# Optimization experiments

Measured on AMD Instinct MI355X. Metric: run time of the kernel, lower is better.

The kernel has to match this reference:

```python
import jax, jax.numpy as jnp
import numpy as np

N_NODES = 50000
N_EDGES = 800000
IN_CH, HID_CH, OUT_CH = 128, 128, 64


def setup_inputs() -> dict:
    key = jax.random.key(0)
    k1, k2, k3, k4 = jax.random.split(key, 4)
    x = jax.random.normal(k1, (N_NODES, IN_CH), dtype=jnp.float32)
    edge_index = jax.random.randint(k2, (2, N_EDGES), 0, N_NODES, dtype=jnp.int64)
    W1 = jax.random.normal(k3, (IN_CH, HID_CH), dtype=jnp.float32) * (1.0 / np.sqrt(IN_CH))
    b1 = jnp.zeros((HID_CH,), dtype=jnp.float32)
    W2 = jax.random.normal(k4, (HID_CH, OUT_CH), dtype=jnp.float32) * (1.0 / np.sqrt(HID_CH))
    b2 = jnp.zeros((OUT_CH,), dtype=jnp.float32)
    return {"x": x, "edge_index": edge_index, "W1": W1, "b1": b1, "W2": W2, "b2": b2}


def _gcn_conv(x, src, dst, norm, W, b, n_nodes):
    # x' = D^-1/2 (A+I) D^-1/2 (x W) + b
    h = x @ W                                        # [N, C_out]
    msg = norm[:, None] * h[src]                     # gather + scale, [E', C_out]
    agg = jax.ops.segment_sum(msg, dst, num_segments=n_nodes)
    return agg + b


def reference(x, edge_index, W1, b1, W2, b2):
    n = x.shape[0]
    # add self loops
    loops = jnp.arange(n, dtype=edge_index.dtype)
    src = jnp.concatenate([edge_index[0], loops])
    dst = jnp.concatenate([edge_index[1], loops])
    # symmetric degree normalization computed on target index
    deg = jax.ops.segment_sum(jnp.ones_like(dst, dtype=x.dtype), dst, num_segments=n)
    dinv = jnp.where(deg > 0, jax.lax.rsqrt(deg), 0.0)
    norm = dinv[src] * dinv[dst]                     # [E']

    h = jax.nn.relu(_gcn_conv(x, src, dst, norm, W1, b1, n))
    logits = _gcn_conv(h, src, dst, norm, W2, b2, n)
    return jax.nn.softmax(logits, axis=1)
```

## Files before the change

### kernel.cpp

```cpp
#include <hip/hip_runtime.h>
#include <hip/hip_fp16.h>


#define SLOT 64
#define NB   49
#define CAP  18432
#define EPB  4096

typedef _Float16 h4 __attribute__((ext_vector_type(4)));
typedef _Float16 h8 __attribute__((ext_vector_type(8)));
typedef float f4 __attribute__((ext_vector_type(4)));

__global__ __launch_bounds__(256) void k_part(const int* __restrict__ ei,
                                              int* __restrict__ bcur,
                                              unsigned int* __restrict__ bkt,
                                              int e) {
    __shared__ int sSrc[EPB];
    __shared__ int sDst[EPB];
    __shared__ int sCnt[64];
    int b0 = blockIdx.x * EPB;
    int cnt = min(EPB, e - b0);
    for (int i = threadIdx.x; i < cnt; i += 256) {
        sSrc[i] = ei[b0 + i];
        sDst[i] = ei[e + b0 + i];
    }
    if (threadIdx.x < 64) sCnt[threadIdx.x] = 0;
    __syncthreads();
    for (int i = threadIdx.x; i < cnt; i += 256)
        atomicAdd(&sCnt[sDst[i] >> 10], 1);
    __syncthreads();
    if (threadIdx.x < 64) {
        int c = sCnt[threadIdx.x];
        int gbase = (c > 0 && threadIdx.x < NB) ? atomicAdd(&bcur[threadIdx.x], c) : 0;
        sCnt[threadIdx.x] = gbase;
    }
    __syncthreads();
    for (int i = threadIdx.x; i < cnt; i += 256) {
        int d = sDst[i];
        int b = d >> 10;
        int pos = atomicAdd(&sCnt[b], 1);
        if (pos < CAP)
            bkt[(size_t)b * CAP + pos] =
                ((unsigned int)(d & 1023) << 16) | (unsigned int)sSrc[i];
    }
}

__global__ __launch_bounds__(256) void k_build(const int* __restrict__ bcur,
                                               const unsigned int* __restrict__ bkt,
                                               unsigned short* __restrict__ csr,
                                               int* __restrict__ deg,
                                               float* __restrict__ dinv, int n) {
    __shared__ unsigned short rows[256 * SLOT];
    __shared__ int cur[256];
    int r = blockIdx.x;
    int b = r >> 2;
    int q = r & 3;
    cur[threadIdx.x] = 0;
    __syncthreads();
    int cnt = min(bcur[b], CAP);
    const unsigned int* bp = bkt + (size_t)b * CAP;
    for (int i = threadIdx.x; i < cnt; i += 256) {
        unsigned int p = bp[i];
        int dl = (int)(p >> 16);
        if ((dl >> 8) == q) {
            int node = dl & 255;
            int pos = atomicAdd(&cur[node], 1);
            if (pos < SLOT) rows[node * SLOT + pos] = (unsigned short)(p & 0xffff);
        }
    }
    __syncthreads();
    int base = r * 256;
    uint4* dst4 = (uint4*)(csr + (size_t)base * SLOT);
    const uint4* src4 = (const uint4*)rows;
    for (int i = threadIdx.x; i < 256 * SLOT / 8; i += 256) dst4[i] = src4[i];
    int node = base + threadIdx.x;
    if (node < n) {
        int c = cur[threadIdx.x];
        deg[node] = c;
        dinv[node] = rsqrtf((float)(c + 1));
    }
}

__global__ __launch_bounds__(256) void k_splitw(const float* __restrict__ W1,
                                                const float* __restrict__ W2,
                                                _Float16* __restrict__ W1p,
                                                _Float16* __restrict__ W2p) {
    int i = blockIdx.x * 256 + threadIdx.x;
    float w; int k, c; _Float16* dst;
    if (i < 16384)      { k = i >> 7, c = i & 127; w = W1[i]; dst = W1p; }
    else if (i < 24576) { int t = i - 16384; k = t >> 6; c = t & 63; w = W2[t]; dst = W2p; }
    else return;
    _Float16 hi = (_Float16)w;
    _Float16 lo = (_Float16)(w - (float)hi);
    int kc = k >> 4, kk = k & 15;
    int l = (kk >> 2) * 16 + (c & 15);
    int j = kk & 3;
    int ct = c >> 4;
    size_t base = ((size_t)(ct * 8 + kc) * 64 + l) * 8 + j;
    dst[base] = hi;
    dst[base + 4] = lo;
}

__global__ __launch_bounds__(256) void k_gemm1(
    const float* __restrict__ X, const _Float16* __restrict__ Wp,
    __half* __restrict__ H, int n)
{
    int w = threadIdx.x >> 6, lane = threadIdx.x & 63;
    int r0 = blockIdx.x * 64 + w * 16;
    int xr = r0 + (lane & 15);
    int xrc = min(xr, n - 1);
    const float* xp = X + (size_t)xrc * 128 + ((lane >> 4) * 4);

    f4 acc[8];
#pragma unroll
    for (int ct = 0; ct < 8; ++ct) acc[ct] = (f4){0.f, 0.f, 0.f, 0.f};

#pragma unroll
    for (int kc = 0; kc < 8; ++kc) {
        float4 xv = *(const float4*)(xp + kc * 16);
        h4 xh, xl;
        xh[0] = (_Float16)xv.x; xh[1] = (_Float16)xv.y;
        xh[2] = (_Float16)xv.z; xh[3] = (_Float16)xv.w;
        xl[0] = (_Float16)(xv.x - (float)xh[0]);
        xl[1] = (_Float16)(xv.y - (float)xh[1]);
        xl[2] = (_Float16)(xv.z - (float)xh[2]);
        xl[3] = (_Float16)(xv.w - (float)xh[3]);
#pragma unroll
        for (int ct = 0; ct < 8; ++ct) {
            h8 wb = ((const h8*)Wp)[(ct * 8 + kc) * 64 + lane];
            h4 wh = {wb[0], wb[1], wb[2], wb[3]};
            h4 wl = {wb[4], wb[5], wb[6], wb[7]};
            acc[ct] = __builtin_amdgcn_mfma_f32_16x16x16f16(wh, xh, acc[ct], 0, 0, 0);
            acc[ct] = __builtin_amdgcn_mfma_f32_16x16x16f16(wl, xh, acc[ct], 0, 0, 0);
            acc[ct] = __builtin_amdgcn_mfma_f32_16x16x16f16(wh, xl, acc[ct], 0, 0, 0);
        }
    }
    if (xr < n) {
        __half* hp = H + (size_t)xr * 128 + (lane >> 4) * 4;
#pragma unroll
        for (int ct = 0; ct < 8; ++ct) {
            h4 o = {(_Float16)acc[ct][0], (_Float16)acc[ct][1],
                    (_Float16)acc[ct][2], (_Float16)acc[ct][3]};
            *(h4*)(hp + ct * 16) = o;
        }
    }
}

__global__ __launch_bounds__(256) void k_agg1(
    const int* __restrict__ deg, const unsigned short* __restrict__ csr,
    const float* __restrict__ dinv, const __half* __restrict__ H,
    const float* __restrict__ b1, float* __restrict__ H1, int n)
{
    int node = blockIdx.x * 4 + (threadIdx.x >> 6);
    if (node >= n) return;
    int lane = threadIdx.x & 63;
    int g = lane >> 4, sub = lane & 15;
    float dd = dinv[node];

    float acc[8];
#pragma unroll
    for (int i = 0; i < 8; ++i) acc[i] = 0.f;

    int beg = node * SLOT;
    int cnt = min(deg[node], SLOT);
    {
        int m = cnt;
        int   s_l = (lane < m) ? (int)csr[beg + lane] : 0;
        float w_l = (lane < m) ? dinv[s_l] * dd : 0.f;
        int iters = (m + 3) >> 2;
#pragma unroll 4
        for (int t = 0; t < iters; ++t) {
            int j = 4 * t + g;
            int   s = __shfl(s_l, j);
            float w = __shfl(w_l, j);
            float4 raw = ((const float4*)(H + (size_t)s * 128))[sub];
            const __half2* h2 = (const __half2*)&raw;
#pragma unroll
            for (int q = 0; q < 4; ++q) {
                float2 v = __half22float2(h2[q]);
                acc[2 * q]     = fmaf(w, v.x, acc[2 * q]);
                acc[2 * q + 1] = fmaf(w, v.y, acc[2 * q + 1]);
            }
        }
    }
#pragma unroll
    for (int i = 0; i < 8; ++i) {
        acc[i] += __shfl_xor(acc[i], 16);
        acc[i] += __shfl_xor(acc[i], 32);
    }
    float4 sraw = ((const float4*)(H + (size_t)node * 128))[sub];
    const __half2* sh2 = (const __half2*)&sraw;
    float sl = dd * dd;
    float4 bb0 = ((const float4*)(b1 + sub * 8))[0];
    float4 bb1 = ((const float4*)(b1 + sub * 8))[1];
    float out[8];
#pragma unroll
    for (int q = 0; q < 4; ++q) {
        float2 v = __half22float2(sh2[q]);
        out[2 * q]     = fmaf(sl, v.x, acc[2 * q]);
        out[2 * q + 1] = fmaf(sl, v.y, acc[2 * q + 1]);
    }
    out[0] += bb0.x; out[1] += bb0.y; out[2] += bb0.z; out[3] += bb0.w;
    out[4] += bb1.x; out[5] += bb1.y; out[6] += bb1.z; out[7] += bb1.w;
#pragma unroll
    for (int i = 0; i < 8; ++i) out[i] = fmaxf(out[i], 0.f);
    float* op = H1 + (size_t)node * 128 + sub * 8;
    if (g == 0) *(float4*)op       = make_float4(out[0], out[1], out[2], out[3]);
    if (g == 1) *(float4*)(op + 4) = make_float4(out[4], out[5], out[6], out[7]);
}

__global__ __launch_bounds__(256) void k_gemm2(
    const float* __restrict__ X, const _Float16* __restrict__ Wp,
    __half* __restrict__ H2, int n)
{
    int w = threadIdx.x >> 6, lane = threadIdx.x & 63;
    int r0 = blockIdx.x * 64 + w * 16;
    int xr = r0 + (lane & 15);
    int xrc = min(xr, n - 1);
    const float* xp = X + (size_t)xrc * 128 + ((lane >> 4) * 4);

    f4 acc[4];
#pragma unroll
    for (int ct = 0; ct < 4; ++ct) acc[ct] = (f4){0.f, 0.f, 0.f, 0.f};

#pragma unroll
    for (int kc = 0; kc < 8; ++kc) {
        float4 xv = *(const float4*)(xp + kc * 16);
        h4 xh, xl;
        xh[0] = (_Float16)xv.x; xh[1] = (_Float16)xv.y;
        xh[2] = (_Float16)xv.z; xh[3] = (_Float16)xv.w;
        xl[0] = (_Float16)(xv.x - (float)xh[0]);
        xl[1] = (_Float16)(xv.y - (float)xh[1]);
        xl[2] = (_Float16)(xv.z - (float)xh[2]);
        xl[3] = (_Float16)(xv.w - (float)xh[3]);
#pragma unroll
        for (int ct = 0; ct < 4; ++ct) {
            h8 wb = ((const h8*)Wp)[(ct * 8 + kc) * 64 + lane];
            h4 wh = {wb[0], wb[1], wb[2], wb[3]};
            h4 wl = {wb[4], wb[5], wb[6], wb[7]};
            acc[ct] = __builtin_amdgcn_mfma_f32_16x16x16f16(wh, xh, acc[ct], 0, 0, 0);
            acc[ct] = __builtin_amdgcn_mfma_f32_16x16x16f16(wl, xh, acc[ct], 0, 0, 0);
            acc[ct] = __builtin_amdgcn_mfma_f32_16x16x16f16(wh, xl, acc[ct], 0, 0, 0);
        }
    }
    if (xr < n) {
        __half* hp = H2 + (size_t)xr * 64 + (lane >> 4) * 4;
#pragma unroll
        for (int ct = 0; ct < 4; ++ct) {
            h4 o = {(_Float16)acc[ct][0], (_Float16)acc[ct][1],
                    (_Float16)acc[ct][2], (_Float16)acc[ct][3]};
            *(h4*)(hp + ct * 16) = o;
        }
    }
}

__global__ __launch_bounds__(256) void k_agg2(
    const int* __restrict__ deg, const unsigned short* __restrict__ csr,
    const float* __restrict__ dinv, const __half* __restrict__ H2,
    const float* __restrict__ b2, float* __restrict__ OUT, int n)
{
    int node = blockIdx.x * 4 + (threadIdx.x >> 6);
    if (node >= n) return;
    int lane = threadIdx.x & 63;
    int g = lane >> 3, sub = lane & 7;
    float dd = dinv[node];

    float acc[8];
#pragma unroll
    for (int i = 0; i < 8; ++i) acc[i] = 0.f;

    int beg = node * SLOT;
    int cnt = min(deg[node], SLOT);
    {
        int m = cnt;
        int   s_l = (lane < m) ? (int)csr[beg + lane] : 0;
        float w_l = (lane < m) ? dinv[s_l] * dd : 0.f;
        int iters = (m + 7) >> 3;
#pragma unroll 4
        for (int t = 0; t < iters; ++t) {
            int j = 8 * t + g;
            int   s = __shfl(s_l, j);
            float w = __shfl(w_l, j);
            float4 raw = ((const float4*)(H2 + (size_t)s * 64))[sub];
            const __half2* h2 = (const __half2*)&raw;
#pragma unroll
            for (int q = 0; q < 4; ++q) {
                float2 v = __half22float2(h2[q]);
                acc[2 * q]     = fmaf(w, v.x, acc[2 * q]);
                acc[2 * q + 1] = fmaf(w, v.y, acc[2 * q + 1]);
            }
        }
    }
#pragma unroll
    for (int i = 0; i < 8; ++i) {
        acc[i] += __shfl_xor(acc[i], 8);
        acc[i] += __shfl_xor(acc[i], 16);
        acc[i] += __shfl_xor(acc[i], 32);
    }
    float4 sraw = ((const float4*)(H2 + (size_t)node * 64))[sub];
    const __half2* sh2 = (const __half2*)&sraw;
    float sl = dd * dd;
    float4 bb0 = ((const float4*)(b2 + sub * 8))[0];
    float4 bb1 = ((const float4*)(b2 + sub * 8))[1];
    float out[8];
#pragma unroll
    for (int q = 0; q < 4; ++q) {
        float2 v = __half22float2(sh2[q]);
        out[2 * q]     = fmaf(sl, v.x, acc[2 * q]);
        out[2 * q + 1] = fmaf(sl, v.y, acc[2 * q + 1]);
    }
    out[0] += bb0.x; out[1] += bb0.y; out[2] += bb0.z; out[3] += bb0.w;
    out[4] += bb1.x; out[5] += bb1.y; out[6] += bb1.z; out[7] += bb1.w;
    float mx = out[0];
#pragma unroll
    for (int i = 1; i < 8; ++i) mx = fmaxf(mx, out[i]);
    mx = fmaxf(mx, __shfl_xor(mx, 1));
    mx = fmaxf(mx, __shfl_xor(mx, 2));
    mx = fmaxf(mx, __shfl_xor(mx, 4));
    float sm = 0.f;
#pragma unroll
    for (int i = 0; i < 8; ++i) { out[i] = expf(out[i] - mx); sm += out[i]; }
    sm += __shfl_xor(sm, 1);
    sm += __shfl_xor(sm, 2);
    sm += __shfl_xor(sm, 4);
    float inv = 1.f / sm;
#pragma unroll
    for (int i = 0; i < 8; ++i) out[i] *= inv;
    float* op = OUT + (size_t)node * 64 + sub * 8;
    if (g == 0) *(float4*)op       = make_float4(out[0], out[1], out[2], out[3]);
    if (g == 1) *(float4*)(op + 4) = make_float4(out[4], out[5], out[6], out[7]);
}

extern "C" void kernel_launch(void* const* d_in, const int* in_sizes, int n_in,
                              void* d_out, int out_size, void* d_ws, size_t ws_size,
                              hipStream_t stream) {
    const float* X  = (const float*)d_in[0];
    const int*   EI = (const int*)d_in[1];
    const float* W1 = (const float*)d_in[2];
    const float* B1 = (const float*)d_in[3];
    const float* W2 = (const float*)d_in[4];
    const float* B2 = (const float*)d_in[5];
    float* OUT = (float*)d_out;

    const int n = in_sizes[0] / 128;
    const int e = in_sizes[1] / 2;

    const int np = (n + 255) & ~255;
    int*            bcur = (int*)d_ws;
    int*            deg  = bcur + 64;
    float*          dinv = (float*)(deg + np);
    unsigned int*   bkt  = (unsigned int*)(dinv + np);
    unsigned short* csr  = (unsigned short*)(bkt + (size_t)NB * CAP);
    _Float16*       W1p  = (_Float16*)(csr + (size_t)np * SLOT);
    _Float16*       W2p  = W1p + 32768;
    __half*         H16  = (__half*)(W2p + 16384);
    float*          H1   = (float*)(H16 + (size_t)np * 128);
    __half*         H2   = (__half*)(H1 + (size_t)n * 128);

    (void)hipMemsetAsync(bcur, 0, 64 * sizeof(int), stream);
    k_splitw<<<96, 256, 0, stream>>>(W1, W2, W1p, W2p);
    k_part<<<(e + EPB - 1) / EPB, 256, 0, stream>>>(EI, bcur, bkt, e);
    k_build<<<np / 256, 256, 0, stream>>>(bcur, bkt, csr, deg, dinv, n);

    k_gemm1<<<(n + 63) / 64, 256, 0, stream>>>(X, W1p, H16, n);
    k_agg1<<<(n + 3) / 4, 256, 0, stream>>>(deg, csr, dinv, H16, B1, H1, n);

    k_gemm2<<<(n + 63) / 64, 256, 0, stream>>>(H1, W2p, H2, n);
    k_agg2<<<(n + 3) / 4, 256, 0, stream>>>(deg, csr, dinv, H2, B2, OUT, n);
}
```

Before: 220.8 us.

## Merge prep kernels, co-launch CSR build with GEMM1, store hidden layer as fp16

Weight splitting is folded into the edge-partition kernel, and the CSR build runs in the same launch as the first GEMM using block-index ranges. This cuts two kernel launches and lets independent work share the GPU. The hidden activations H1 are now written as fp16 instead of fp32, which halves that traffic. GEMM2 therefore drops the low-part correction of X and uses 2 MFMAs per tile instead of 3. The cost is lower precision in the second layer's input, which may push error closer to tolerance.

```diff
diff --git a/kernel.cpp b/kernel.cpp
--- a/kernel.cpp
+++ b/kernel.cpp
@@ -11,137 +11,138 @@
 typedef _Float16 h8 __attribute__((ext_vector_type(8)));
 typedef float f4 __attribute__((ext_vector_type(4)));
 
-__global__ __launch_bounds__(256) void k_part(const int* __restrict__ ei,
+__global__ __launch_bounds__(256) void k_prep(const int* __restrict__ ei,
                                               int* __restrict__ bcur,
                                               unsigned int* __restrict__ bkt,
-                                              int e) {
+                                              const float* __restrict__ W1,
+                                              const float* __restrict__ W2,
+                                              _Float16* __restrict__ W1p,
+                                              _Float16* __restrict__ W2p,
+                                              int e, int pb) {
     __shared__ int sSrc[EPB];
     __shared__ int sDst[EPB];
     __shared__ int sCnt[64];
-    int b0 = blockIdx.x * EPB;
-    int cnt = min(EPB, e - b0);
-    for (int i = threadIdx.x; i < cnt; i += 256) {
-        sSrc[i] = ei[b0 + i];
-        sDst[i] = ei[e + b0 + i];
-    }
-    if (threadIdx.x < 64) sCnt[threadIdx.x] = 0;
-    __syncthreads();
-    for (int i = threadIdx.x; i < cnt; i += 256)
-        atomicAdd(&sCnt[sDst[i] >> 10], 1);
-    __syncthreads();
-    if (threadIdx.x < 64) {
-        int c = sCnt[threadIdx.x];
-        int gbase = (c > 0 && threadIdx.x < NB) ? atomicAdd(&bcur[threadIdx.x], c) : 0;
-        sCnt[threadIdx.x] = gbase;
-    }
-    __syncthreads();
-    for (int i = threadIdx.x; i < cnt; i += 256) {
-        int d = sDst[i];
-        int b = d >> 10;
-        int pos = atomicAdd(&sCnt[b], 1);
-        if (pos < CAP)
-            bkt[(size_t)b * CAP + pos] =
-                ((unsigned int)(d & 1023) << 16) | (unsigned int)sSrc[i];
-    }
-}
-
-__global__ __launch_bounds__(256) void k_build(const int* __restrict__ bcur,
-                                               const unsigned int* __restrict__ bkt,
-                                               unsigned short* __restrict__ csr,
-                                               int* __restrict__ deg,
-                                               float* __restrict__ dinv, int n) {
+    if (blockIdx.x < pb) {
+        int b0 = blockIdx.x * EPB;
+        int cnt = min(EPB, e - b0);
+        for (int i = threadIdx.x; i < cnt; i += 256) {
+            sSrc[i] = ei[b0 + i];
+            sDst[i] = ei[e + b0 + i];
+        }
+        if (threadIdx.x < 64) sCnt[threadIdx.x] = 0;
+        __syncthreads();
+        for (int i = threadIdx.x; i < cnt; i += 256)
+            atomicAdd(&sCnt[sDst[i] >> 10], 1);
+        __syncthreads();
+        if (threadIdx.x < 64) {
+            int c = sCnt[threadIdx.x];
+            int gbase = (c > 0 && threadIdx.x < NB) ? atomicAdd(&bcur[threadIdx.x], c) : 0;
+            sCnt[threadIdx.x] = gbase;
+        }
+        __syncthreads();
+        for (int i = threadIdx.x; i < cnt; i += 256) {
+            int d = sDst[i];
+            int b = d >> 10;
+            int pos = atomicAdd(&sCnt[b], 1);
+            if (pos < CAP)
+                bkt[(size_t)b * CAP + pos] =
+                    ((unsigned int)(d & 1023) << 16) | (unsigned int)sSrc[i];
+        }
+    } else {
+        int i = (blockIdx.x - pb) * 256 + threadIdx.x;
+        float w; int k, c; _Float16* dst;
+        if (i < 16384)      { k = i >> 7, c = i & 127; w = W1[i]; dst = W1p; }
+        else if (i < 24576) { int t = i - 16384; k = t >> 6; c = t & 63; w = W2[t]; dst = W2p; }
+        else return;
+        _Float16 hi = (_Float16)w;
+        _Float16 lo = (_Float16)(w - (float)hi);
+        int kc = k >> 4, kk = k & 15;
+        int l = (kk >> 2) * 16 + (c & 15);
+        int j = kk & 3;
+        int ct = c >> 4;
+        size_t base = ((size_t)(ct * 8 + kc) * 64 + l) * 8 + j;
+        dst[base] = hi;
+        dst[base + 4] = lo;
+    }
+}
+
+__global__ __launch_bounds__(256) void k_main1(
+    const int* __restrict__ bcur, const unsigned int* __restrict__ bkt,
+    unsigned short* __restrict__ csr, int* __restrict__ deg,
+    float* __restrict__ dinv,
+    const float* __restrict__ X, const _Float16* __restrict__ Wp,
+    __half* __restrict__ H, int n, int bb)
+{
     __shared__ unsigned short rows[256 * SLOT];
     __shared__ int cur[256];
-    int r = blockIdx.x;
-    int b = r >> 2;
-    int q = r & 3;
-    cur[threadIdx.x] = 0;
-    __syncthreads();
-    int cnt = min(bcur[b], CAP);
-    const unsigned int* bp = bkt + (size_t)b * CAP;
-    for (int i = threadIdx.x; i < cnt; i += 256) {
-        unsigned int p = bp[i];
-        int dl = (int)(p >> 16);
-        if ((dl >> 8) == q) {
-            int node = dl & 255;
-            int pos = atomicAdd(&cur[node], 1);
-            if (pos < SLOT) rows[node * SLOT + pos] = (unsigned short)(p & 0xffff);
-        }
-    }
-    __syncthreads();
-    int base = r * 256;
-    uint4* dst4 = (uint4*)(csr + (size_t)base * SLOT);
-    const uint4* src4 = (const uint4*)rows;
-    for (int i = threadIdx.x; i < 256 * SLOT / 8; i += 256) dst4[i] = src4[i];
-    int node = base + threadIdx.x;
-    if (node < n) {
-        int c = cur[threadIdx.x];
-        deg[node] = c;
-        dinv[node] = rsqrtf((float)(c + 1));
-    }
-}
-
-__global__ __launch_bounds__(256) void k_splitw(const float* __restrict__ W1,
-                                                const float* __restrict__ W2,
-                                                _Float16* __restrict__ W1p,
-                                                _Float16* __restrict__ W2p) {
-    int i = blockIdx.x * 256 + threadIdx.x;
-    float w; int k, c; _Float16* dst;
-    if (i < 16384)      { k = i >> 7, c = i & 127; w = W1[i]; dst = W1p; }
-    else if (i < 24576) { int t = i - 16384; k = t >> 6; c = t & 63; w = W2[t]; dst = W2p; }
-    else return;
-    _Float16 hi = (_Float16)w;
-    _Float16 lo = (_Float16)(w - (float)hi);
-    int kc = k >> 4, kk = k & 15;
-    int l = (kk >> 2) * 16 + (c & 15);
-    int j = kk & 3;
-    int ct = c >> 4;
-    size_t base = ((size_t)(ct * 8 + kc) * 64 + l) * 8 + j;
-    dst[base] = hi;
-    dst[base + 4] = lo;
-}
-
-__global__ __launch_bounds__(256) void k_gemm1(
-    const float* __restrict__ X, const _Float16* __restrict__ Wp,
-    __half* __restrict__ H, int n)
-{
-    int w = threadIdx.x >> 6, lane = threadIdx.x & 63;
-    int r0 = blockIdx.x * 64 + w * 16;
-    int xr = r0 + (lane & 15);
-    int xrc = min(xr, n - 1);
-    const float* xp = X + (size_t)xrc * 128 + ((lane >> 4) * 4);
-
-    f4 acc[8];
-#pragma unroll
-    for (int ct = 0; ct < 8; ++ct) acc[ct] = (f4){0.f, 0.f, 0.f, 0.f};
-
-#pragma unroll
-    for (int kc = 0; kc < 8; ++kc) {
-        float4 xv = *(const float4*)(xp + kc * 16);
-        h4 xh, xl;
-        xh[0] = (_Float16)xv.x; xh[1] = (_Float16)xv.y;
-        xh[2] = (_Float16)xv.z; xh[3] = (_Float16)xv.w;
-        xl[0] = (_Float16)(xv.x - (float)xh[0]);
-        xl[1] = (_Float16)(xv.y - (float)xh[1]);
-        xl[2] = (_Float16)(xv.z - (float)xh[2]);
-        xl[3] = (_Float16)(xv.w - (float)xh[3]);
-#pragma unroll
-        for (int ct = 0; ct < 8; ++ct) {
-            h8 wb = ((const h8*)Wp)[(ct * 8 + kc) * 64 + lane];
-            h4 wh = {wb[0], wb[1], wb[2], wb[3]};
-            h4 wl = {wb[4], wb[5], wb[6], wb[7]};
-            acc[ct] = __builtin_amdgcn_mfma_f32_16x16x16f16(wh, xh, acc[ct], 0, 0, 0);
-            acc[ct] = __builtin_amdgcn_mfma_f32_16x16x16f16(wl, xh, acc[ct], 0, 0, 0);
-            acc[ct] = __builtin_amdgcn_mfma_f32_16x16x16f16(wh, xl, acc[ct], 0, 0, 0);
-        }
-    }
-    if (xr < n) {
-        __half* hp = H + (size_t)xr * 128 + (lane >> 4) * 4;
-#pragma unroll
-        for (int ct = 0; ct < 8; ++ct) {
-            h4 o = {(_Float16)acc[ct][0], (_Float16)acc[ct][1],
-                    (_Float16)acc[ct][2], (_Float16)acc[ct][3]};
-            *(h4*)(hp + ct * 16) = o;
+    if (blockIdx.x < bb) {
+        int r = blockIdx.x;
+        int b = r >> 2;
+        int q = r & 3;
+        cur[threadIdx.x] = 0;
+        __syncthreads();
+        int cnt = min(bcur[b], CAP);
+        const unsigned int* bp = bkt + (size_t)b * CAP;
+        for (int i = threadIdx.x; i < cnt; i += 256) {
+            unsigned int p = bp[i];
+            int dl = (int)(p >> 16);
+            if ((dl >> 8) == q) {
+                int node = dl & 255;
+                int pos = atomicAdd(&cur[node], 1);
+                if (pos < SLOT) rows[node * SLOT + pos] = (unsigned short)(p & 0xffff);
+            }
+        }
+        __syncthreads();
+        int base = r * 256;
+        uint4* dst4 = (uint4*)(csr + (size_t)base * SLOT);
+        const uint4* src4 = (const uint4*)rows;
+        for (int i = threadIdx.x; i < 256 * SLOT / 8; i += 256) dst4[i] = src4[i];
+        int node = base + threadIdx.x;
+        if (node < n) {
+            int c = cur[threadIdx.x];
+            deg[node] = c;
+            dinv[node] = rsqrtf((float)(c + 1));
+        }
+    } else {
+        int blk = blockIdx.x - bb;
+        int w = threadIdx.x >> 6, lane = threadIdx.x & 63;
+        int r0 = blk * 64 + w * 16;
+        int xr = r0 + (lane & 15);
+        int xrc = min(xr, n - 1);
+        const float* xp = X + (size_t)xrc * 128 + ((lane >> 4) * 4);
+
+        f4 acc[8];
+#pragma unroll
+        for (int ct = 0; ct < 8; ++ct) acc[ct] = (f4){0.f, 0.f, 0.f, 0.f};
+
+#pragma unroll
+        for (int kc = 0; kc < 8; ++kc) {
+            float4 xv = *(const float4*)(xp + kc * 16);
+            h4 xh, xl;
+            xh[0] = (_Float16)xv.x; xh[1] = (_Float16)xv.y;
+            xh[2] = (_Float16)xv.z; xh[3] = (_Float16)xv.w;
+            xl[0] = (_Float16)(xv.x - (float)xh[0]);
+            xl[1] = (_Float16)(xv.y - (float)xh[1]);
+            xl[2] = (_Float16)(xv.z - (float)xh[2]);
+            xl[3] = (_Float16)(xv.w - (float)xh[3]);
+#pragma unroll
+            for (int ct = 0; ct < 8; ++ct) {
+                h8 wb = ((const h8*)Wp)[(ct * 8 + kc) * 64 + lane];
+                h4 wh = {wb[0], wb[1], wb[2], wb[3]};
+                h4 wl = {wb[4], wb[5], wb[6], wb[7]};
+                acc[ct] = __builtin_amdgcn_mfma_f32_16x16x16f16(wh, xh, acc[ct], 0, 0, 0);
+                acc[ct] = __builtin_amdgcn_mfma_f32_16x16x16f16(wl, xh, acc[ct], 0, 0, 0);
+                acc[ct] = __builtin_amdgcn_mfma_f32_16x16x16f16(wh, xl, acc[ct], 0, 0, 0);
+            }
+        }
+        if (xr < n) {
+            __half* hp = H + (size_t)xr * 128 + (lane >> 4) * 4;
+#pragma unroll
+            for (int ct = 0; ct < 8; ++ct) {
+                h4 o = {(_Float16)acc[ct][0], (_Float16)acc[ct][1],
+                        (_Float16)acc[ct][2], (_Float16)acc[ct][3]};
+                *(h4*)(hp + ct * 16) = o;
+            }
         }
     }
 }
@@ -149,7 +150,7 @@
 __global__ __launch_bounds__(256) void k_agg1(
     const int* __restrict__ deg, const unsigned short* __restrict__ csr,
     const float* __restrict__ dinv, const __half* __restrict__ H,
-    const float* __restrict__ b1, float* __restrict__ H1, int n)
+    const float* __restrict__ b1, __half* __restrict__ H1, int n)
 {
     int node = blockIdx.x * 4 + (threadIdx.x >> 6);
     if (node >= n) return;
@@ -202,22 +203,23 @@
     }
     out[0] += bb0.x; out[1] += bb0.y; out[2] += bb0.z; out[3] += bb0.w;
     out[4] += bb1.x; out[5] += bb1.y; out[6] += bb1.z; out[7] += bb1.w;
-#pragma unroll
-    for (int i = 0; i < 8; ++i) out[i] = fmaxf(out[i], 0.f);
-    float* op = H1 + (size_t)node * 128 + sub * 8;
-    if (g == 0) *(float4*)op       = make_float4(out[0], out[1], out[2], out[3]);
-    if (g == 1) *(float4*)(op + 4) = make_float4(out[4], out[5], out[6], out[7]);
+    if (g == 0) {
+        h8 o;
+#pragma unroll
+        for (int i = 0; i < 8; ++i) o[i] = (_Float16)fmaxf(out[i], 0.f);
+        *(h8*)(H1 + (size_t)node * 128 + sub * 8) = o;
+    }
 }
 
 __global__ __launch_bounds__(256) void k_gemm2(
-    const float* __restrict__ X, const _Float16* __restrict__ Wp,
+    const __half* __restrict__ Xh, const _Float16* __restrict__ Wp,
     __half* __restrict__ H2, int n)
 {
     int w = threadIdx.x >> 6, lane = threadIdx.x & 63;
     int r0 = blockIdx.x * 64 + w * 16;
     int xr = r0 + (lane & 15);
     int xrc = min(xr, n - 1);
-    const float* xp = X + (size_t)xrc * 128 + ((lane >> 4) * 4);
+    const _Float16* xp = (const _Float16*)Xh + (size_t)xrc * 128 + ((lane >> 4) * 4);
 
     f4 acc[4];
 #pragma unroll
@@ -225,14 +227,7 @@
 
 #pragma unroll
     for (int kc = 0; kc < 8; ++kc) {
-        float4 xv = *(const float4*)(xp + kc * 16);
-        h4 xh, xl;
-        xh[0] = (_Float16)xv.x; xh[1] = (_Float16)xv.y;
-        xh[2] = (_Float16)xv.z; xh[3] = (_Float16)xv.w;
-        xl[0] = (_Float16)(xv.x - (float)xh[0]);
-        xl[1] = (_Float16)(xv.y - (float)xh[1]);
-        xl[2] = (_Float16)(xv.z - (float)xh[2]);
-        xl[3] = (_Float16)(xv.w - (float)xh[3]);
+        h4 xh = *(const h4*)(xp + kc * 16);
 #pragma unroll
         for (int ct = 0; ct < 4; ++ct) {
             h8 wb = ((const h8*)Wp)[(ct * 8 + kc) * 64 + lane];
@@ -240,7 +235,6 @@
             h4 wl = {wb[4], wb[5], wb[6], wb[7]};
             acc[ct] = __builtin_amdgcn_mfma_f32_16x16x16f16(wh, xh, acc[ct], 0, 0, 0);
             acc[ct] = __builtin_amdgcn_mfma_f32_16x16x16f16(wl, xh, acc[ct], 0, 0, 0);
-            acc[ct] = __builtin_amdgcn_mfma_f32_16x16x16f16(wh, xl, acc[ct], 0, 0, 0);
         }
     }
     if (xr < n) {
@@ -354,17 +348,18 @@
     _Float16*       W1p  = (_Float16*)(csr + (size_t)np * SLOT);
     _Float16*       W2p  = W1p + 32768;
     __half*         H16  = (__half*)(W2p + 16384);
-    float*          H1   = (float*)(H16 + (size_t)np * 128);
-    __half*         H2   = (__half*)(H1 + (size_t)n * 128);
+    __half*         H1   = (__half*)(H16 + (size_t)np * 128);
+    __half*         H2   = H1 + (size_t)np * 128;
+
+    const int pb = (e + EPB - 1) / EPB;
+    const int bb = np / 256;
+    const int gb = (n + 63) / 64;
 
     (void)hipMemsetAsync(bcur, 0, 64 * sizeof(int), stream);
-    k_splitw<<<96, 256, 0, stream>>>(W1, W2, W1p, W2p);
-    k_part<<<(e + EPB - 1) / EPB, 256, 0, stream>>>(EI, bcur, bkt, e);
-    k_build<<<np / 256, 256, 0, stream>>>(bcur, bkt, csr, deg, dinv, n);
-
-    k_gemm1<<<(n + 63) / 64, 256, 0, stream>>>(X, W1p, H16, n);
+    k_prep<<<pb + 96, 256, 0, stream>>>(EI, bcur, bkt, W1, W2, W1p, W2p, e, pb);
+    k_main1<<<bb + gb, 256, 0, stream>>>(bcur, bkt, csr, deg, dinv,
+                                         X, W1p, H16, n, bb);
     k_agg1<<<(n + 3) / 4, 256, 0, stream>>>(deg, csr, dinv, H16, B1, H1, n);
-
-    k_gemm2<<<(n + 63) / 64, 256, 0, stream>>>(H1, W2p, H2, n);
+    k_gemm2<<<gb, 256, 0, stream>>>(H1, W2p, H2, n);
     k_agg2<<<(n + 3) / 4, 256, 0, stream>>>(deg, csr, dinv, H2, B2, OUT, n);
 }
```

After: 194.1 us. -12.1%, faster.
